# Optimization experiments

Hardware: AMD Instinct MI355X
Metric: run time of the kernel (lower is better)

## Reference

```python
import jax, jax.numpy as jnp
import numpy as np

MARGIN = 0.3
EPS_DIST = 1e-12   # clamp before sqrt, as in torch source
EPS_PAIR = 1e-6    # torch F.pairwise_distance eps added to the difference


def setup_inputs() -> dict:
    key = jax.random.key(0)
    k1, k2 = jax.random.split(key)
    n, d = 8192, 256
    inputs = jax.random.normal(k1, (n, d), dtype=jnp.float32)
    positive = jax.random.normal(k2, (n, d), dtype=jnp.float32)
    return {"inputs": inputs, "positive": positive}


def reference(inputs, positive):
    # Pairwise Euclidean distances: ||xi||^2 + ||xj||^2 - 2 xi.xj
    sq = jnp.sum(inputs * inputs, axis=1)                      # [n]
    dist = sq[:, None] + sq[None, :] - 2.0 * (inputs @ inputs.T)  # [n, n]
    dist = jnp.sqrt(jnp.clip(dist, EPS_DIST))
    # 3rd-smallest per row (index 2 of argsort); row i's smallest is itself.
    _, idx3 = jax.lax.top_k(-dist, 3)                          # [n, 3]
    negative = inputs[idx3[:, 2]]                              # [n, d] gather
    # TripletMarginLoss(margin, p=2): mean(relu(d(a,p) - d(a,n) + margin))
    d_ap = jnp.linalg.norm(inputs - positive + EPS_PAIR, axis=1)
    d_an = jnp.linalg.norm(inputs - negative + EPS_PAIR, axis=1)
    return jnp.mean(jnp.maximum(d_ap - d_an + MARGIN, 0.0))
```

## Files before the change

kernel.cpp:

```cpp
#include <hip/hip_runtime.h>
#include <math.h>

#define N 8192
#define D 256
#define NCH 32
#define RB 256
#define RT 4
#define CHUNK (N / NCH)
#define NCT (CHUNK / 16)

constexpr float MARGIN = 0.3f;
constexpr float EPS_PAIR = 1e-6f;
constexpr float BIAS = 512.0f;

typedef float f32x4 __attribute__((ext_vector_type(4)));
typedef int   i32x4 __attribute__((ext_vector_type(4)));
typedef int   i32x8 __attribute__((ext_vector_type(8)));

__device__ __forceinline__ void load_lds16(const void* g, void* l) {
  __builtin_amdgcn_global_load_lds((const __attribute__((address_space(1))) void*)g,
                                   (__attribute__((address_space(3))) void*)l, 16, 0, 0);
}

__device__ __forceinline__ void top2merge(unsigned& v1, unsigned& v2,
                                          unsigned w1, unsigned w2) {
  unsigned mx = v1 > w1 ? v1 : w1;
  v1 = v1 < w1 ? v1 : w1;
  unsigned mn = v2 < w2 ? v2 : w2;
  v2 = mx < mn ? mx : mn;
}

__global__ void prep_kernel(const float* __restrict__ in, char* __restrict__ A8,
                            float* __restrict__ sqh) {
  int row  = blockIdx.x * 4 + (threadIdx.x >> 6);
  int lane = threadIdx.x & 63;
  float4 v = ((const float4*)(in + (size_t)row * D))[lane];
  int w = 0;
  w = __builtin_amdgcn_cvt_pk_fp8_f32(v.x, v.y, w, false);
  w = __builtin_amdgcn_cvt_pk_fp8_f32(v.z, v.w, w, true);
  *(int*)(A8 + (size_t)row * D + lane * 4) = w;
  float s = v.x * v.x + v.y * v.y + v.z * v.z + v.w * v.w;
#pragma unroll
  for (int m = 32; m; m >>= 1) s += __shfl_xor(s, m);
  if (lane == 0) sqh[row] = -0.5f * (s + BIAS);
}

__global__ __launch_bounds__(256, 3) void neighbor_kernel(
    const char* __restrict__ A8, const float* __restrict__ sqh,
    uint2* __restrict__ pp) {
  __shared__ __attribute__((aligned(16))) char ldsB[2][4096];
  __shared__ float ldsSq[CHUNK];

  const int t = threadIdx.x;
  const int lane = t & 63;
  const int wave = t >> 6;
  const int rowBase = blockIdx.x * RB + wave * 64;
  const int colBase = blockIdx.y * CHUNK;

  const int lrow = lane & 15;
  const int lkg  = lane >> 4;

  i32x8 afrag[RT][2];
#pragma unroll
  for (int rt = 0; rt < RT; ++rt) {
    const char* arow = A8 + (size_t)(rowBase + rt * 16 + lrow) * D;
#pragma unroll
    for (int ks = 0; ks < 2; ++ks)
      afrag[rt][ks] = *(const i32x8*)(arow + ks * 128 + lkg * 32);
  }

  for (int i = t; i < CHUNK; i += 256) ldsSq[i] = sqh[colBase + i];

  int dsoff[4];
#pragma unroll
  for (int ks = 0; ks < 2; ++ks)
#pragma unroll
    for (int h = 0; h < 2; ++h)
      dsoff[ks * 2 + h] = lrow * 256 + ((ks * 128 + lkg * 32 + h * 16) ^ ((lrow & 7) << 4));

  auto stage = [&](int buf, int ct) {
    int p = wave * 1024 + lane * 16;
    int r = p >> 8;
    int o = p & 255;
    const char* src = A8 + (size_t)(colBase + ct * 16 + r) * 256 + (o ^ ((r & 7) << 4));
    load_lds16(src, &ldsB[buf][p]);
  };

  unsigned v1[RT][4], v2[RT][4];
#pragma unroll
  for (int rt = 0; rt < RT; ++rt)
#pragma unroll
    for (int q = 0; q < 4; ++q) { v1[rt][q] = 0xFFFFFFFFu; v2[rt][q] = 0xFFFFFFFFu; }

  stage(0, 0);
  __syncthreads();

  auto body = [&](int ct, int buf) {
    if (ct + 1 < NCT) stage(buf ^ 1, ct + 1);

    const float sqv = ldsSq[ct * 16 + lrow];
    f32x4 acc[RT];
#pragma unroll
    for (int rt = 0; rt < RT; ++rt) acc[rt] = (f32x4){sqv, sqv, sqv, sqv};

    const char* bt = ldsB[buf];
#pragma unroll
    for (int ks = 0; ks < 2; ++ks) {
      i32x4 lo = *(const i32x4*)(bt + dsoff[ks * 2]);
      i32x4 hi = *(const i32x4*)(bt + dsoff[ks * 2 + 1]);
      i32x8 bfrag = __builtin_shufflevector(lo, hi, 0, 1, 2, 3, 4, 5, 6, 7);
#pragma unroll
      for (int rt = 0; rt < RT; ++rt)
        acc[rt] = __builtin_amdgcn_mfma_scale_f32_16x16x128_f8f6f4(
            afrag[rt][ks], bfrag, acc[rt], 0, 0,
            0, 0x7F7F7F7F, 0, 0x7F7F7F7F);
    }

    const int j = colBase + ct * 16 + lrow;
#pragma unroll
    for (int rt = 0; rt < RT; ++rt) {
      const bool diag = (colBase + ct * 16) == (rowBase + rt * 16);
#pragma unroll
      for (int q = 0; q < 4; ++q) {
        unsigned p = (__float_as_uint(acc[rt][q]) & 0xFFFFE000u) | (unsigned)j;
        if (diag) p = (lrow == lkg * 4 + q) ? 0xFFFFFFFFu : p;
        unsigned nv1 = v1[rt][q] < p ? v1[rt][q] : p;
        unsigned mx  = p > v1[rt][q] ? p : v1[rt][q];
        v2[rt][q] = v2[rt][q] < mx ? v2[rt][q] : mx;
        v1[rt][q] = nv1;
      }
    }
    __syncthreads();
  };

  for (int ct = 0; ct < NCT; ct += 2) {
    body(ct, 0);
    body(ct + 1, 1);
  }

#pragma unroll
  for (int rt = 0; rt < RT; ++rt) {
#pragma unroll
    for (int q = 0; q < 4; ++q) {
      unsigned a1 = v1[rt][q], a2 = v2[rt][q];
#pragma unroll
      for (int m = 1; m < 16; m <<= 1) {
        unsigned w1 = (unsigned)__shfl_xor((int)a1, m);
        unsigned w2 = (unsigned)__shfl_xor((int)a2, m);
        top2merge(a1, a2, w1, w2);
      }
      if (lrow == 0) {
        int ig = rowBase + rt * 16 + lkg * 4 + q;
        pp[(size_t)blockIdx.y * N + ig] = make_uint2(a1, a2);
      }
    }
  }
}

__global__ void finish_kernel(const float* __restrict__ A, const float* __restrict__ P,
                              const uint2* __restrict__ pp, float* __restrict__ rowLoss) {
  int row  = blockIdx.x * 4 + (threadIdx.x >> 6);
  int lane = threadIdx.x & 63;

  uint2 pr = pp[(size_t)(lane & 31) * N + row];
  unsigned a1 = pr.x, a2 = pr.y;
#pragma unroll
  for (int m = 1; m < 32; m <<= 1) {
    unsigned w1 = (unsigned)__shfl_xor((int)a1, m);
    unsigned w2 = (unsigned)__shfl_xor((int)a2, m);
    top2merge(a1, a2, w1, w2);
  }
  int nr = (int)(a2 & 0x1FFFu);

  float4 av = ((const float4*)(A + (size_t)row * D))[lane];
  float4 pv = ((const float4*)(P + (size_t)row * D))[lane];
  float4 gv = ((const float4*)(A + (size_t)nr  * D))[lane];
  float dap = 0.f, dan = 0.f, x;
  x = av.x - pv.x + EPS_PAIR; dap += x * x;
  x = av.y - pv.y + EPS_PAIR; dap += x * x;
  x = av.z - pv.z + EPS_PAIR; dap += x * x;
  x = av.w - pv.w + EPS_PAIR; dap += x * x;
  x = av.x - gv.x + EPS_PAIR; dan += x * x;
  x = av.y - gv.y + EPS_PAIR; dan += x * x;
  x = av.z - gv.z + EPS_PAIR; dan += x * x;
  x = av.w - gv.w + EPS_PAIR; dan += x * x;
#pragma unroll
  for (int m = 32; m; m >>= 1) {
    dap += __shfl_xor(dap, m);
    dan += __shfl_xor(dan, m);
  }
  if (lane == 0)
    rowLoss[row] = fmaxf(sqrtf(dap) - sqrtf(dan) + MARGIN, 0.f);
}

__global__ void reduce_kernel(const float* __restrict__ rowLoss, float* __restrict__ out) {
  __shared__ float smem[256];
  int t = threadIdx.x;
  float s = 0.f;
  for (int i = t; i < N; i += 256) s += rowLoss[i];
  smem[t] = s;
  __syncthreads();
  for (int stride = 128; stride; stride >>= 1) {
    if (t < stride) smem[t] += smem[t + stride];
    __syncthreads();
  }
  if (t == 0) out[0] = smem[0] * (1.0f / (float)N);
}

extern "C" void kernel_launch(void* const* d_in, const int* in_sizes, int n_in,
                              void* d_out, int out_size, void* d_ws, size_t ws_size,
                              hipStream_t stream) {
  const float* inputs   = (const float*)d_in[0];
  const float* positive = (const float*)d_in[1];
  float* out = (float*)d_out;

  char*  A8      = (char*)d_ws;
  float* sqh     = (float*)(A8 + (size_t)N * D);
  uint2* pp      = (uint2*)(sqh + N);
  float* rowLoss = (float*)(pp + (size_t)NCH * N);

  prep_kernel<<<N / 4, 256, 0, stream>>>(inputs, A8, sqh);
  neighbor_kernel<<<dim3(N / RB, NCH), 256, 0, stream>>>(A8, sqh, pp);
  finish_kernel<<<N / 4, 256, 0, stream>>>(inputs, positive, pp, rowLoss);
  reduce_kernel<<<1, 256, 0, stream>>>(rowLoss, out);
}
```

Before: 55.62 us.

## Stage entire column chunk into LDS once and drop per-tile barriers

```diff
diff --git a/kernel.cpp b/kernel.cpp
--- a/kernel.cpp
+++ b/kernel.cpp
@@ -45,10 +45,10 @@
   if (lane == 0) sqh[row] = -0.5f * (s + BIAS);
 }
 
-__global__ __launch_bounds__(256, 3) void neighbor_kernel(
+__global__ __launch_bounds__(256, 2) void neighbor_kernel(
     const char* __restrict__ A8, const float* __restrict__ sqh,
     uint2* __restrict__ pp) {
-  __shared__ __attribute__((aligned(16))) char ldsB[2][4096];
+  __shared__ __attribute__((aligned(16))) char ldsB[CHUNK * 256];
   __shared__ float ldsSq[CHUNK];
 
   const int t = threadIdx.x;
@@ -60,6 +60,17 @@
   const int lrow = lane & 15;
   const int lkg  = lane >> 4;
 
+  {
+    int r0 = t >> 4;
+    int o0 = (t & 15) * 16;
+    const char* src = A8 + (size_t)(colBase + r0) * 256 + (o0 ^ ((r0 & 7) << 4));
+#pragma unroll
+    for (int it = 0; it < 16; ++it) {
+      load_lds16(src, &ldsB[it * 4096 + t * 16]);
+      src += 4096;
+    }
+  }
+
   i32x8 afrag[RT][2];
 #pragma unroll
   for (int rt = 0; rt < RT; ++rt) {
@@ -78,32 +89,22 @@
     for (int h = 0; h < 2; ++h)
       dsoff[ks * 2 + h] = lrow * 256 + ((ks * 128 + lkg * 32 + h * 16) ^ ((lrow & 7) << 4));
 
-  auto stage = [&](int buf, int ct) {
-    int p = wave * 1024 + lane * 16;
-    int r = p >> 8;
-    int o = p & 255;
-    const char* src = A8 + (size_t)(colBase + ct * 16 + r) * 256 + (o ^ ((r & 7) << 4));
-    load_lds16(src, &ldsB[buf][p]);
-  };
-
   unsigned v1[RT][4], v2[RT][4];
 #pragma unroll
   for (int rt = 0; rt < RT; ++rt)
 #pragma unroll
     for (int q = 0; q < 4; ++q) { v1[rt][q] = 0xFFFFFFFFu; v2[rt][q] = 0xFFFFFFFFu; }
 
-  stage(0, 0);
   __syncthreads();
 
-  auto body = [&](int ct, int buf) {
-    if (ct + 1 < NCT) stage(buf ^ 1, ct + 1);
-
+#pragma unroll 2
+  for (int ct = 0; ct < NCT; ++ct) {
+    const char* bt = ldsB + ct * 4096;
     const float sqv = ldsSq[ct * 16 + lrow];
     f32x4 acc[RT];
 #pragma unroll
     for (int rt = 0; rt < RT; ++rt) acc[rt] = (f32x4){sqv, sqv, sqv, sqv};
 
-    const char* bt = ldsB[buf];
 #pragma unroll
     for (int ks = 0; ks < 2; ++ks) {
       i32x4 lo = *(const i32x4*)(bt + dsoff[ks * 2]);
@@ -130,12 +131,6 @@
         v1[rt][q] = nv1;
       }
     }
-    __syncthreads();
-  };
-
-  for (int ct = 0; ct < NCT; ct += 2) {
-    body(ct, 0);
-    body(ct + 1, 1);
   }
 
 #pragma unroll
```

Measured after the change: 54.56 us. About the same (-1.9%).
